# Performance work log

Measured on AMD Instinct MI355X. Metric: run time of the kernel, lower is better.

Reference implementation:

```python
import jax, jax.numpy as jnp
import numpy as np


def _freq_downsample(x, sf):
    # torch: stack(chunk(dim=2), 4) -> cat(chunk(dim=3), 4) -> mean(-1) -> repeat(1,1,sf,sf)
    # equivalent: mean over the sf x sf grid of contiguous blocks, then tile back.
    B, C, H, W = x.shape
    m = x.reshape(B, C, sf, H // sf, sf, W // sf).mean(axis=(2, 4))
    return jnp.tile(m, (1, 1, sf, sf))


def setup_inputs() -> dict:
    key = jax.random.key(0)
    k1, k2, k3 = jax.random.split(key, 3)
    shape = (4, 3, 256, 256)
    return {
        "STy": jax.random.normal(k1, shape, dtype=jnp.float32),
        "Fk_real": jax.random.normal(k2, shape, dtype=jnp.float32),
        "Fk_imag": jax.random.normal(k3, shape, dtype=jnp.float32),
        "sf": 2,
    }


def _forward(STy, Fk_real, Fk_imag, sf, num_iters=50, alpha=1e-6, gam=0.1):
    fft2 = lambda a: jnp.fft.fft2(a, axes=(-2, -1))
    ifft2 = lambda a: jnp.fft.ifft2(a, axes=(-2, -1))

    Fk = jax.lax.complex(Fk_real, Fk_imag)          # complex64 OTF
    FkC = jnp.conj(Fk)
    Fk2 = Fk_real ** 2 + Fk_imag ** 2               # |Fk|^2, real

    FSTy = fft2(STy)
    Fr = FkC * FSTy / (_freq_downsample(Fk2, sf) + alpha)
    pred = ifft2(Fr).real

    # finite-difference stencils DH = [1,-1] horizontal, DV vertical
    DH = jnp.zeros_like(pred).at[..., 0, 0].set(1.0).at[..., 0, 1].set(-1.0)
    DV = jnp.zeros_like(pred).at[..., 0, 0].set(1.0).at[..., 1, 0].set(-1.0)
    FDH, FDV = fft2(DH), fft2(DV)
    FDHC, FDVC = jnp.conj(FDH), jnp.conj(FDV)
    FD2 = jnp.abs(FDV) ** 2 + jnp.abs(FDH) ** 2 + 1e-8  # real

    # loop-invariant terms (identical math to recomputing each iteration)
    den = _freq_downsample(Fk2 / FD2, sf) + alpha
    FkFSTy = FkC * FSTy

    def body(carry, k):
        pred, x_old, t_old, U1, U2, D1, D2 = carry
        gam_k = gam * jnp.exp2(-k / num_iters)      # gam * 0.5 ** (k/num_iters)
        Fr = FkFSTy + alpha * (FDHC * fft2(U1 - D1) + FDVC * fft2(U2 - D2))
        Fr = (Fr - FkC * _freq_downsample(Fk * Fr / FD2, sf) / den) / (alpha * FD2)
        x_new = ifft2(Fr).real
        t_new = (1.0 + jnp.sqrt(1.0 + 4.0 * t_old ** 2)) / 2.0
        pred = x_new + (t_old - 1.0) / t_new * (x_new - x_old)
        DHr = ifft2(Fr * FDH).real
        DVr = ifft2(Fr * FDV).real
        NU1, NU2 = DHr + D1, DVr + D2
        NU = jnp.sqrt(NU1 ** 2 + NU2 ** 2 + 1e-8)
        A = jnp.maximum(0.0, NU - gam_k) + 1e-8
        A = A / (A + gam_k)                         # soft-threshold magnitude shrink
        U1n, U2n = A * NU1, A * NU2
        return (pred, x_new, t_new, U1n, U2n, D1 + DHr - U1n, D2 + DVr - U2n), None

    carry0 = (pred, pred, jnp.float32(1.0), pred, pred,
              jnp.zeros_like(pred), jnp.zeros_like(pred))
    ks = jnp.arange(num_iters, dtype=jnp.float32)
    (pred, *_), _ = jax.lax.scan(body, carry0, ks)
    return pred


def reference(STy, Fk_real, Fk_imag, sf):
    return _forward(STy, Fk_real, Fk_imag, sf)
```

## Files before the change

kernel.cpp:

```cpp
#include <hip/hip_runtime.h>
#include <math.h>

#define NIMG 12
#define NSZ 256
#define HWSZ 65536
#define NBLK 768

struct GBar { unsigned cnt; unsigned gen; };

__device__ __forceinline__ void gsync(GBar* b)
{
  __syncthreads();
  if (threadIdx.x == 0) {
    __threadfence();
    unsigned g = __hip_atomic_load(&b->gen, __ATOMIC_RELAXED, __HIP_MEMORY_SCOPE_AGENT);
    unsigned a = __hip_atomic_fetch_add(&b->cnt, 1u, __ATOMIC_ACQ_REL, __HIP_MEMORY_SCOPE_AGENT);
    if (a == NBLK - 1u) {
      __hip_atomic_store(&b->cnt, 0u, __ATOMIC_RELAXED, __HIP_MEMORY_SCOPE_AGENT);
      __hip_atomic_store(&b->gen, g + 1u, __ATOMIC_RELEASE, __HIP_MEMORY_SCOPE_AGENT);
    } else {
      while (__hip_atomic_load(&b->gen, __ATOMIC_ACQUIRE, __HIP_MEMORY_SCOPE_AGENT) == g)
        __builtin_amdgcn_s_sleep(2);
    }
    __threadfence();
  }
  __syncthreads();
}

__device__ __forceinline__ void fft256g(float2* A, float2* B, const float2* tw, int lane,
                                        float dir, bool active)
{
  float2* src = A;
  float2* dst = B;
  int m = 1;
#pragma unroll
  for (int s = 0; s < 8; ++s) {
    __syncthreads();
    if (active) {
#pragma unroll
      for (int h = 0; h < 2; ++h) {
        int b = lane + (h << 6);
        int k = b & (m - 1);
        int jm = b - k;
        float2 a = src[b];
        float2 c = src[b + 128];
        float2 w = tw[jm];
        float wr = w.x, wi = dir * w.y;
        float ex = a.x - c.x, ey = a.y - c.y;
        dst[2 * jm + k]     = make_float2(a.x + c.x, a.y + c.y);
        dst[2 * jm + k + m] = make_float2(ex * wr - ey * wi, ex * wi + ey * wr);
      }
    }
    float2* t = src; src = dst; dst = t;
    m <<= 1;
  }
  __syncthreads();
}
__device__ __forceinline__ void fft256(float2* A, float2* B, const float2* tw, int lane, float dir)
{
  fft256g(A, B, tw, lane, dir, true);
}

__device__ __forceinline__ void make_tw(float2* tw, int t)
{
  float s, c;
  sincospif((float)t * (1.0f / 128.0f), &s, &c);
  tw[t] = make_float2(c, s);
}

__device__ __forceinline__ double fdval(const float2* tw, int k)
{
  return 2.0 - 2.0 * (double)tw[k].x;
}

__global__ __launch_bounds__(256, 3) void k_mega(const float* __restrict__ sty,
                                                 const float* __restrict__ fkr,
                                                 const float* __restrict__ fki,
                                                 float2* __restrict__ WG,
                                                 float2* __restrict__ WF,
                                                 float2* __restrict__ FkF,
                                                 float* __restrict__ denq,
                                                 float* D1a, float* D2a,
                                                 float* D1b, float* D2b,
                                                 float* __restrict__ x49,
                                                 float* __restrict__ out,
                                                 float cmom, GBar* bar)
{
  __shared__ float2 tw[256];
  __shared__ float2 bufA[6][256];
  __shared__ float2 bufB[6][256];
  __shared__ float aL[5][256];
  __shared__ float bL[5][256];
  __shared__ float dsA[2][128];
  __shared__ double2 Ml[2][128];

  int t = threadIdx.x;
  make_tw(tw, t);
  int bid = blockIdx.x;
  int n = bid >> 6;
  int sr = bid & 63;
  int r0 = sr << 2;
  int j0 = sr << 1;
  int w = t >> 6, lane = t & 63;
  const float sc = 1.0f / 65536.0f;
  int gcw = j0 + (w & 1) + ((w >> 1) << 7);

  {
    const float* src = sty + (size_t)n * HWSZ + (size_t)(r0 + w) * NSZ;
#pragma unroll
    for (int q = 0; q < 4; ++q) { int j = lane + (q << 6); bufA[w][j] = make_float2(src[j], 0.f); }
    fft256(bufA[w], bufB[w], tw, lane, -1.f);
    float2* dst = WG + (size_t)n * HWSZ + (size_t)(r0 + w) * NSZ;
#pragma unroll
    for (int q = 0; q < 4; ++q) { int j = lane + (q << 6); dst[j] = bufA[w][j]; }
  }
  gsync(bar);

  {
    float2* WGn = WG + (size_t)n * HWSZ;
#pragma unroll
    for (int q = 0; q < 4; ++q) { int u = lane + (q << 6); bufA[w][u] = WGn[(size_t)u * NSZ + gcw]; }
    fft256(bufA[w], bufB[w], tw, lane, -1.f);
#pragma unroll
    for (int c = 0; c < 4; ++c) {
      int u = t;
      int gc = j0 + (c & 1) + ((c >> 1) << 7);
      size_t idx = (size_t)n * HWSZ + (size_t)u * NSZ + gc;
      float kr = fkr[idx], ki = fki[idx];
      float2 f = bufA[c][u];
      float2 kf = make_float2(kr * f.x + ki * f.y, kr * f.y - ki * f.x);
      FkF[idx] = kf;
      bufA[c][u] = kf;
    }
    __syncthreads();
    {
      int u0 = t & 127, p = t >> 7;
      double s1 = 0.0, s2 = 0.0;
#pragma unroll
      for (int s = 0; s < 4; ++s) {
        int u = u0 + ((s & 1) << 7);
        int c = p + ((s >> 1) << 1);
        int gc = j0 + (c & 1) + ((c >> 1) << 7);
        size_t idx = (size_t)n * HWSZ + (size_t)u * NSZ + gc;
        double kr = fkr[idx], ki = fki[idx];
        double k2 = kr * kr + ki * ki;
        double fd2 = fdval(tw, u) + fdval(tw, gc) + 1e-8;
        s1 += k2;
        s2 += k2 / fd2;
      }
      denq[(size_t)n * 16384 + (size_t)u0 * 128 + (j0 + p)] = (float)(s2 * 0.25 + 1e-6);
      dsA[p][u0] = (float)(s1 * 0.25 + 1e-6);
    }
    __syncthreads();
#pragma unroll
    for (int c = 0; c < 4; ++c) {
      int u = t;
      float d = dsA[c & 1][u & 127];
      float2 kf = bufA[c][u];
      bufA[c][u] = make_float2(kf.x / d, kf.y / d);
    }
    fft256(bufA[w], bufB[w], tw, lane, +1.f);
    float2* WFn = WF + (size_t)n * HWSZ;
#pragma unroll
    for (int q = 0; q < 4; ++q) { int u = lane + (q << 6); WFn[(size_t)u * NSZ + gcw] = bufA[w][u]; }
  }
  gsync(bar);

  for (int k = 0; k < 50; ++k) {
    float gamp = (k >= 1) ? (float)(0.1 * exp2(-(double)(k - 1) / 50.0)) : 0.f;
    const float *D1p, *D2p; float *D1w, *D2w;
    if (k & 1) { D1p = D1a; D2p = D2a; D1w = D1b; D2w = D2b; }
    else       { D1p = D1b; D2p = D2b; D1w = D1a; D2w = D2a; }

    {
      int gr = (r0 + w - 1) & 255;
      const float2* srcW = WF + (size_t)n * HWSZ + (size_t)gr * NSZ;
#pragma unroll
      for (int q = 0; q < 4; ++q) { int j = lane + (q << 6); bufA[w][j] = srcW[j]; }
      fft256(bufA[w], bufB[w], tw, lane, +1.f);
    }
    {
      bool act = (w < 2);
      int e = 4 + (w & 1);
      int gr = (r0 + e - 1) & 255;
      if (act) {
        const float2* srcW = WF + (size_t)n * HWSZ + (size_t)gr * NSZ;
#pragma unroll
        for (int q = 0; q < 4; ++q) { int j = lane + (q << 6); bufA[e][j] = srcW[j]; }
      }
      fft256g(bufA[e], bufB[e], tw, lane, +1.f, act);
    }
    for (int e = 1; e <= 5; ++e) {
      int gr = (r0 + e - 1) & 255;
      int j = t, jm1 = (j - 1) & 255;
      float xc = bufA[e][j].x * sc;
      size_t idx = (size_t)n * HWSZ + (size_t)gr * NSZ + j;
      if (k == 49 && e <= 4) x49[idx] = xc;
      float a, b;
      if (k == 0) {
        a = xc; b = xc;
      } else {
        float xl = bufA[e][jm1].x * sc;
        float xu = bufA[e - 1][j].x * sc;
        float dhr = xc - xl;
        float dvr = xc - xu;
        float d1 = D1p[idx], d2 = D2p[idx];
        float nu1 = dhr + d1, nu2 = dvr + d2;
        float nu = sqrtf(nu1 * nu1 + nu2 * nu2 + 1e-8f);
        float A = fmaxf(0.f, nu - gamp) + 1e-8f;
        A = A / (A + gamp);
        float u1 = A * nu1, u2 = A * nu2;
        float d1v = d1 + dhr - u1;
        float d2v = d2 + dvr - u2;
        if (e <= 4) { D1w[idx] = d1v; D2w[idx] = d2v; }
        a = u1 - d1v; b = u2 - d2v;
      }
      aL[e - 1][j] = a;
      bL[e - 1][j] = b;
    }
    __syncthreads();
    {
#pragma unroll
      for (int q = 0; q < 4; ++q) {
        int j = lane + (q << 6);
        int jp1 = (j + 1) & 255;
        float g = aL[w][j] - aL[w][jp1] + bL[w][j] - bL[w + 1][j];
        bufA[w][j] = make_float2(g, 0.f);
      }
      fft256(bufA[w], bufB[w], tw, lane, -1.f);
      float2* dst = WG + (size_t)n * HWSZ + (size_t)(r0 + w) * NSZ;
#pragma unroll
      for (int q = 0; q < 4; ++q) { int j = lane + (q << 6); dst[j] = bufA[w][j]; }
    }
    gsync(bar);

    {
      float2* WGn = WG + (size_t)n * HWSZ;
#pragma unroll
      for (int q = 0; q < 4; ++q) { int u = lane + (q << 6); bufA[w][u] = WGn[(size_t)u * NSZ + gcw]; }
      fft256(bufA[w], bufB[w], tw, lane, -1.f);
#pragma unroll
      for (int c = 0; c < 4; ++c) {
        int u = t;
        int gc = j0 + (c & 1) + ((c >> 1) << 7);
        size_t idx = (size_t)n * HWSZ + (size_t)u * NSZ + gc;
        float2 kf = FkF[idx];
        float2 fg = bufA[c][u];
        bufA[c][u] = make_float2(kf.x + 1e-6f * fg.x, kf.y + 1e-6f * fg.y);
      }
      __syncthreads();
      {
        int u0 = t & 127, p = t >> 7;
        double sx = 0.0, sy = 0.0;
#pragma unroll
        for (int s = 0; s < 4; ++s) {
          int u = u0 + ((s & 1) << 7);
          int c = p + ((s >> 1) << 1);
          int gc = j0 + (c & 1) + ((c >> 1) << 7);
          size_t idx = (size_t)n * HWSZ + (size_t)u * NSZ + gc;
          float2 f1 = bufA[c][u];
          double kr = fkr[idx], ki = fki[idx];
          double fd2 = fdval(tw, u) + fdval(tw, gc) + 1e-8;
          sx += (kr * (double)f1.x - ki * (double)f1.y) / fd2;
          sy += (kr * (double)f1.y + ki * (double)f1.x) / fd2;
        }
        Ml[p][u0] = make_double2(sx * 0.25, sy * 0.25);
      }
      __syncthreads();
#pragma unroll
      for (int c = 0; c < 4; ++c) {
        int u = t;
        int gc = j0 + (c & 1) + ((c >> 1) << 7);
        size_t idx = (size_t)n * HWSZ + (size_t)u * NSZ + gc;
        float2 f1 = bufA[c][u];
        double2 m = Ml[c & 1][u & 127];
        double den = (double)denq[(size_t)n * 16384 + (size_t)(u & 127) * 128 + (j0 + (c & 1))];
        double kr = fkr[idx], ki = fki[idx];
        double px = (kr * m.x + ki * m.y) / den;
        double py = (kr * m.y - ki * m.x) / den;
        double fd2 = fdval(tw, u) + fdval(tw, gc) + 1e-8;
        double s2 = 1.0 / (1e-6 * fd2);
        bufA[c][u] = make_float2((float)(((double)f1.x - px) * s2),
                                 (float)(((double)f1.y - py) * s2));
      }
      fft256(bufA[w], bufB[w], tw, lane, +1.f);
      float2* WFn = WF + (size_t)n * HWSZ;
#pragma unroll
      for (int q = 0; q < 4; ++q) { int u = lane + (q << 6); WFn[(size_t)u * NSZ + gcw] = bufA[w][u]; }
    }
    gsync(bar);
  }

  {
    const float2* srcW = WF + (size_t)n * HWSZ + (size_t)(r0 + w) * NSZ;
#pragma unroll
    for (int q = 0; q < 4; ++q) { int j = lane + (q << 6); bufA[w][j] = srcW[j]; }
    fft256(bufA[w], bufB[w], tw, lane, +1.f);
    size_t base = (size_t)n * HWSZ + (size_t)(r0 + w) * NSZ;
#pragma unroll
    for (int q = 0; q < 4; ++q) {
      int j = lane + (q << 6);
      float v = bufA[w][j].x * sc;
      out[base + j] = v + cmom * (v - x49[base + j]);
    }
  }
}

__global__ __launch_bounds__(256) void k_rowfwd_sty(const float* __restrict__ sty,
                                                    float2* __restrict__ Wb)
{
  __shared__ float2 tw[256];
  __shared__ float2 bufA[4][256];
  __shared__ float2 bufB[4][256];
  int t = threadIdx.x;
  make_tw(tw, t);
  int n = blockIdx.x >> 6;
  int r0 = (blockIdx.x & 63) << 2;
  int w = t >> 6, lane = t & 63;
  const float* src = sty + (size_t)n * HWSZ + (size_t)(r0 + w) * NSZ;
#pragma unroll
  for (int q = 0; q < 4; ++q) { int j = lane + (q << 6); bufA[w][j] = make_float2(src[j], 0.f); }
  fft256(bufA[w], bufB[w], tw, lane, -1.f);
  float2* dst = Wb + (size_t)n * HWSZ + (size_t)(r0 + w) * NSZ;
#pragma unroll
  for (int q = 0; q < 4; ++q) { int j = lane + (q << 6); dst[j] = bufA[w][j]; }
}

__global__ __launch_bounds__(256) void k_colsetup(float2* __restrict__ Wb,
                                                  float2* __restrict__ FkF,
                                                  const float* __restrict__ fkr,
                                                  const float* __restrict__ fki,
                                                  float* __restrict__ denq)
{
  __shared__ float2 tw[256];
  __shared__ float2 bufA[4][256];
  __shared__ float2 bufB[4][256];
  __shared__ float dsA[2][128];
  int t = threadIdx.x;
  make_tw(tw, t);
  int n = blockIdx.x >> 6;
  int j0 = (blockIdx.x & 63) << 1;
  int w = t >> 6, lane = t & 63;
  int gcw = j0 + (w & 1) + ((w >> 1) << 7);
  float2* Wn = Wb + (size_t)n * HWSZ;
#pragma unroll
  for (int q = 0; q < 4; ++q) { int u = lane + (q << 6); bufA[w][u] = Wn[(size_t)u * NSZ + gcw]; }
  fft256(bufA[w], bufB[w], tw, lane, -1.f);
#pragma unroll
  for (int c = 0; c < 4; ++c) {
    int u = t;
    int gc = j0 + (c & 1) + ((c >> 1) << 7);
    size_t idx = (size_t)n * HWSZ + (size_t)u * NSZ + gc;
    float kr = fkr[idx], ki = fki[idx];
    float2 f = bufA[c][u];
    float2 kf = make_float2(kr * f.x + ki * f.y, kr * f.y - ki * f.x);
    FkF[idx] = kf;
    bufA[c][u] = kf;
  }
  __syncthreads();
  {
    int u0 = t & 127, p = t >> 7;
    double s1 = 0.0, s2 = 0.0;
#pragma unroll
    for (int s = 0; s < 4; ++s) {
      int u = u0 + ((s & 1) << 7);
      int c = p + ((s >> 1) << 1);
      int gc = j0 + (c & 1) + ((c >> 1) << 7);
      size_t idx = (size_t)n * HWSZ + (size_t)u * NSZ + gc;
      double kr = fkr[idx], ki = fki[idx];
      double k2 = kr * kr + ki * ki;
      double fd2 = fdval(tw, u) + fdval(tw, gc) + 1e-8;
      s1 += k2;
      s2 += k2 / fd2;
    }
    denq[(size_t)n * 16384 + (size_t)u0 * 128 + (j0 + p)] = (float)(s2 * 0.25 + 1e-6);
    dsA[p][u0] = (float)(s1 * 0.25 + 1e-6);
  }
  __syncthreads();
#pragma unroll
  for (int c = 0; c < 4; ++c) {
    int u = t;
    float d = dsA[c & 1][u & 127];
    float2 kf = bufA[c][u];
    bufA[c][u] = make_float2(kf.x / d, kf.y / d);
  }
  fft256(bufA[w], bufB[w], tw, lane, +1.f);
#pragma unroll
  for (int q = 0; q < 4; ++q) { int u = lane + (q << 6); Wn[(size_t)u * NSZ + gcw] = bufA[w][u]; }
}

__global__ __launch_bounds__(256) void k_spatial_rowfwd(const float* __restrict__ x,
                                                        const float* __restrict__ D1p,
                                                        const float* __restrict__ D2p,
                                                        float* __restrict__ D1n,
                                                        float* __restrict__ D2n,
                                                        float2* __restrict__ Wb,
                                                        float gamp, int firstIter)
{
  __shared__ float2 tw[256];
  __shared__ float aL[5][256];
  __shared__ float bL[5][256];
  __shared__ float2 bufA[4][256];
  __shared__ float2 bufB[4][256];
  int t = threadIdx.x;
  make_tw(tw, t);
  int n = blockIdx.x >> 6;
  int r0 = (blockIdx.x & 63) << 2;
  const float* xn = x + (size_t)n * HWSZ;
  for (int rr = 0; rr < 5; ++rr) {
    int i = (r0 + rr) & 255;
    int im1 = (i - 1) & 255;
    int j = t;
    int jm1 = (j - 1) & 255;
    float xc = xn[(size_t)i * NSZ + j];
    float a, b;
    if (firstIter) {
      a = xc; b = xc;
    } else {
      float dhr = xc - xn[(size_t)i * NSZ + jm1];
      float dvr = xc - xn[(size_t)im1 * NSZ + j];
      size_t idx = (size_t)n * HWSZ + (size_t)i * NSZ + j;
      float d1 = D1p[idx], d2 = D2p[idx];
      float nu1 = dhr + d1, nu2 = dvr + d2;
      float nu = sqrtf(nu1 * nu1 + nu2 * nu2 + 1e-8f);
      float A = fmaxf(0.f, nu - gamp) + 1e-8f;
      A = A / (A + gamp);
      float u1 = A * nu1, u2 = A * nu2;
      float d1v = d1 + dhr - u1;
      float d2v = d2 + dvr - u2;
      if (rr < 4) { D1n[idx] = d1v; D2n[idx] = d2v; }
      a = u1 - d1v; b = u2 - d2v;
    }
    aL[rr][j] = a;
    bL[rr][j] = b;
  }
  __syncthreads();
  int w = t >> 6, lane = t & 63;
#pragma unroll
  for (int q = 0; q < 4; ++q) {
    int j = lane + (q << 6);
    int jp1 = (j + 1) & 255;
    float g = aL[w][j] - aL[w][jp1] + bL[w][j] - bL[w + 1][j];
    bufA[w][j] = make_float2(g, 0.f);
  }
  fft256(bufA[w], bufB[w], tw, lane, -1.f);
  float2* dst = Wb + (size_t)n * HWSZ + (size_t)(r0 + w) * NSZ;
#pragma unroll
  for (int q = 0; q < 4; ++q) { int j = lane + (q << 6); dst[j] = bufA[w][j]; }
}

__global__ __launch_bounds__(256) void k_colphase(float2* __restrict__ Wb,
                                                  const float2* __restrict__ FkF,
                                                  const float* __restrict__ fkr,
                                                  const float* __restrict__ fki,
                                                  const float* __restrict__ denq)
{
  __shared__ float2 tw[256];
  __shared__ float2 bufA[4][256];
  __shared__ float2 bufB[4][256];
  __shared__ double2 Ml[2][128];
  int t = threadIdx.x;
  make_tw(tw, t);
  int n = blockIdx.x >> 6;
  int j0 = (blockIdx.x & 63) << 1;
  int w = t >> 6, lane = t & 63;
  int gcw = j0 + (w & 1) + ((w >> 1) << 7);
  float2* Wn = Wb + (size_t)n * HWSZ;
#pragma unroll
  for (int q = 0; q < 4; ++q) { int u = lane + (q << 6); bufA[w][u] = Wn[(size_t)u * NSZ + gcw]; }
  fft256(bufA[w], bufB[w], tw, lane, -1.f);
#pragma unroll
  for (int c = 0; c < 4; ++c) {
    int u = t;
    int gc = j0 + (c & 1) + ((c >> 1) << 7);
    size_t idx = (size_t)n * HWSZ + (size_t)u * NSZ + gc;
    float2 kf = FkF[idx];
    float2 fg = bufA[c][u];
    bufA[c][u] = make_float2(kf.x + 1e-6f * fg.x, kf.y + 1e-6f * fg.y);
  }
  __syncthreads();
  {
    int u0 = t & 127, p = t >> 7;
    double sx = 0.0, sy = 0.0;
#pragma unroll
    for (int s = 0; s < 4; ++s) {
      int u = u0 + ((s & 1) << 7);
      int c = p + ((s >> 1) << 1);
      int gc = j0 + (c & 1) + ((c >> 1) << 7);
      size_t idx = (size_t)n * HWSZ + (size_t)u * NSZ + gc;
      float2 f1 = bufA[c][u];
      double kr = fkr[idx], ki = fki[idx];
      double fd2 = fdval(tw, u) + fdval(tw, gc) + 1e-8;
      sx += (kr * (double)f1.x - ki * (double)f1.y) / fd2;
      sy += (kr * (double)f1.y + ki * (double)f1.x) / fd2;
    }
    Ml[p][u0] = make_double2(sx * 0.25, sy * 0.25);
  }
  __syncthreads();
#pragma unroll
  for (int c = 0; c < 4; ++c) {
    int u = t;
    int gc = j0 + (c & 1) + ((c >> 1) << 7);
    size_t idx = (size_t)n * HWSZ + (size_t)u * NSZ + gc;
    float2 f1 = bufA[c][u];
    double2 m = Ml[c & 1][u & 127];
    double den = (double)denq[(size_t)n * 16384 + (size_t)(u & 127) * 128 + (j0 + (c & 1))];
    double kr = fkr[idx], ki = fki[idx];
    double px = (kr * m.x + ki * m.y) / den;
    double py = (kr * m.y - ki * m.x) / den;
    double fd2 = fdval(tw, u) + fdval(tw, gc) + 1e-8;
    double s2 = 1.0 / (1e-6 * fd2);
    bufA[c][u] = make_float2((float)(((double)f1.x - px) * s2),
                             (float)(((double)f1.y - py) * s2));
  }
  fft256(bufA[w], bufB[w], tw, lane, +1.f);
#pragma unroll
  for (int q = 0; q < 4; ++q) { int u = lane + (q << 6); Wn[(size_t)u * NSZ + gcw] = bufA[w][u]; }
}

__global__ __launch_bounds__(256) void k_rowinv(const float2* __restrict__ Wb,
                                                float* __restrict__ xout,
                                                const float* __restrict__ xold,
                                                float* __restrict__ pred,
                                                float cmom, int isLast)
{
  __shared__ float2 tw[256];
  __shared__ float2 bufA[4][256];
  __shared__ float2 bufB[4][256];
  int t = threadIdx.x;
  make_tw(tw, t);
  int n = blockIdx.x >> 6;
  int r0 = (blockIdx.x & 63) << 2;
  int w = t >> 6, lane = t & 63;
  const float2* src = Wb + (size_t)n * HWSZ + (size_t)(r0 + w) * NSZ;
#pragma unroll
  for (int q = 0; q < 4; ++q) { int j = lane + (q << 6); bufA[w][j] = src[j]; }
  fft256(bufA[w], bufB[w], tw, lane, +1.f);
  size_t base = (size_t)n * HWSZ + (size_t)(r0 + w) * NSZ;
#pragma unroll
  for (int q = 0; q < 4; ++q) {
    int j = lane + (q << 6);
    float v = bufA[w][j].x * (1.0f / 65536.0f);
    xout[base + j] = v;
    if (isLast) pred[base + j] = v + cmom * (v - xold[base + j]);
  }
}

extern "C" void kernel_launch(void* const* d_in, const int* in_sizes, int n_in,
                              void* d_out, int out_size, void* d_ws, size_t ws_size,
                              hipStream_t stream)
{
  (void)in_sizes; (void)n_in; (void)out_size; (void)ws_size;
  const float* STy = (const float*)d_in[0];
  const float* fkr = (const float*)d_in[1];
  const float* fki = (const float*)d_in[2];
  float* out = (float*)d_out;

  char* p = (char*)d_ws;
  const size_t cplx = (size_t)NIMG * HWSZ * sizeof(float2);
  const size_t realb = (size_t)NIMG * HWSZ * sizeof(float);
  float2* WG  = (float2*)p; p += cplx;
  float2* WF  = (float2*)p; p += cplx;
  float2* FkF = (float2*)p; p += cplx;
  float* denq = (float*)p;  p += (size_t)NIMG * 16384 * sizeof(float);
  float* D1a = (float*)p;   p += realb;
  float* D2a = (float*)p;   p += realb;
  float* D1b = (float*)p;   p += realb;
  float* D2b = (float*)p;   p += realb;
  float* xA  = (float*)p;   p += realb;
  float* xB  = (float*)p;   p += realb;
  GBar* bar  = (GBar*)p;    p += 64;

  double t_old = 1.0, cm = 0.0;
  for (int k = 0; k < 50; ++k) {
    double t_new = (1.0 + sqrt(1.0 + 4.0 * t_old * t_old)) * 0.5;
    if (k == 49) cm = (t_old - 1.0) / t_new;
    t_old = t_new;
  }

  int maxb = 0;
  hipError_t oe = hipOccupancyMaxActiveBlocksPerMultiprocessor(&maxb, k_mega, 256, 0);
  bool coop = (oe == hipSuccess && maxb >= 3);

  hipMemsetAsync(D1a, 0, 2 * realb, stream);

  dim3 grid(NBLK), blk(256);
  if (coop) {
    hipMemsetAsync(bar, 0, sizeof(GBar), stream);
    k_mega<<<grid, blk, 0, stream>>>(STy, fkr, fki, WG, WF, FkF, denq,
                                     D1a, D2a, D1b, D2b, xA, out, (float)cm, bar);
  } else {
    float2* Wb = WG;
    float* x0 = xA; float* x1 = xB;
    k_rowfwd_sty<<<grid, blk, 0, stream>>>(STy, Wb);
    k_colsetup<<<grid, blk, 0, stream>>>(Wb, FkF, fkr, fki, denq);
    k_rowinv<<<grid, blk, 0, stream>>>(Wb, x0, x0, out, 0.f, 0);
    double to = 1.0;
    for (int k = 0; k < 50; ++k) {
      float gamp = (k >= 1) ? (float)(0.1 * exp2(-(double)(k - 1) / 50.0)) : 0.f;
      const float* xk = (k & 1) ? x1 : x0;
      float* xn = (k & 1) ? x0 : x1;
      const float* D1p = (k & 1) ? D1a : D1b;
      const float* D2p = (k & 1) ? D2a : D2b;
      float* D1w = (k & 1) ? D1b : D1a;
      float* D2w = (k & 1) ? D2b : D2a;
      k_spatial_rowfwd<<<grid, blk, 0, stream>>>(xk, D1p, D2p, D1w, D2w, Wb, gamp, (k == 0) ? 1 : 0);
      k_colphase<<<grid, blk, 0, stream>>>(Wb, FkF, fkr, fki, denq);
      double tn = (1.0 + sqrt(1.0 + 4.0 * to * to)) * 0.5;
      int isLast = (k == 49) ? 1 : 0;
      float cmom = (float)((to - 1.0) / tn);
      k_rowinv<<<grid, blk, 0, stream>>>(Wb, xn, xk, out, isLast ? cmom : 0.f, isLast);
      to = tn;
    }
  }
}
```

Baseline: 2.499 ms.

## Replace global grid barrier with per-image flag barriers

Swaps the single grid-wide counter barrier for a per-image barrier. Each of the 64 blocks working on an image publishes a generation flag, and one wavefront polls all 64 flags of that image. Images no longer wait on each other, and contention on a single atomic counter goes away. This relies on each image's data dependencies being confined to its own 64 blocks, and it adds polling traffic on 64 flags per block.

```diff
diff --git a/kernel.cpp b/kernel.cpp
--- a/kernel.cpp
+++ b/kernel.cpp
@@ -6,23 +6,20 @@
 #define HWSZ 65536
 #define NBLK 768
 
-struct GBar { unsigned cnt; unsigned gen; };
-
-__device__ __forceinline__ void gsync(GBar* b)
-{
-  __syncthreads();
-  if (threadIdx.x == 0) {
-    __threadfence();
-    unsigned g = __hip_atomic_load(&b->gen, __ATOMIC_RELAXED, __HIP_MEMORY_SCOPE_AGENT);
-    unsigned a = __hip_atomic_fetch_add(&b->cnt, 1u, __ATOMIC_ACQ_REL, __HIP_MEMORY_SCOPE_AGENT);
-    if (a == NBLK - 1u) {
-      __hip_atomic_store(&b->cnt, 0u, __ATOMIC_RELAXED, __HIP_MEMORY_SCOPE_AGENT);
-      __hip_atomic_store(&b->gen, g + 1u, __ATOMIC_RELEASE, __HIP_MEMORY_SCOPE_AGENT);
-    } else {
-      while (__hip_atomic_load(&b->gen, __ATOMIC_ACQUIRE, __HIP_MEMORY_SCOPE_AGENT) == g)
-        __builtin_amdgcn_s_sleep(2);
-    }
-    __threadfence();
+__device__ __forceinline__ void isync(unsigned* flags, int base, int sr, unsigned gen)
+{
+  __syncthreads();
+  int t = threadIdx.x;
+  if (t < 64) {
+    if (t == 0) {
+      __builtin_amdgcn_fence(__ATOMIC_RELEASE, "agent");
+      __hip_atomic_store(&flags[base + sr], gen, __ATOMIC_RELAXED, __HIP_MEMORY_SCOPE_AGENT);
+    }
+    unsigned v;
+    do {
+      v = __hip_atomic_load(&flags[base + t], __ATOMIC_RELAXED, __HIP_MEMORY_SCOPE_AGENT);
+    } while (__any(v < gen));
+    __builtin_amdgcn_fence(__ATOMIC_ACQUIRE, "agent");
   }
   __syncthreads();
 }
@@ -84,7 +81,7 @@
                                                  float* D1b, float* D2b,
                                                  float* __restrict__ x49,
                                                  float* __restrict__ out,
-                                                 float cmom, GBar* bar)
+                                                 float cmom, unsigned* flags)
 {
   __shared__ float2 tw[256];
   __shared__ float2 bufA[6][256];
@@ -99,11 +96,13 @@
   int bid = blockIdx.x;
   int n = bid >> 6;
   int sr = bid & 63;
+  int fbase = n << 6;
   int r0 = sr << 2;
   int j0 = sr << 1;
   int w = t >> 6, lane = t & 63;
   const float sc = 1.0f / 65536.0f;
   int gcw = j0 + (w & 1) + ((w >> 1) << 7);
+  unsigned gen = 0;
 
   {
     const float* src = sty + (size_t)n * HWSZ + (size_t)(r0 + w) * NSZ;
@@ -114,7 +113,7 @@
 #pragma unroll
     for (int q = 0; q < 4; ++q) { int j = lane + (q << 6); dst[j] = bufA[w][j]; }
   }
-  gsync(bar);
+  isync(flags, fbase, sr, ++gen);
 
   {
     float2* WGn = WG + (size_t)n * HWSZ;
@@ -164,7 +163,7 @@
 #pragma unroll
     for (int q = 0; q < 4; ++q) { int u = lane + (q << 6); WFn[(size_t)u * NSZ + gcw] = bufA[w][u]; }
   }
-  gsync(bar);
+  isync(flags, fbase, sr, ++gen);
 
   for (int k = 0; k < 50; ++k) {
     float gamp = (k >= 1) ? (float)(0.1 * exp2(-(double)(k - 1) / 50.0)) : 0.f;
@@ -232,7 +231,7 @@
 #pragma unroll
       for (int q = 0; q < 4; ++q) { int j = lane + (q << 6); dst[j] = bufA[w][j]; }
     }
-    gsync(bar);
+    isync(flags, fbase, sr, ++gen);
 
     {
       float2* WGn = WG + (size_t)n * HWSZ;
@@ -288,7 +287,7 @@
 #pragma unroll
       for (int q = 0; q < 4; ++q) { int u = lane + (q << 6); WFn[(size_t)u * NSZ + gcw] = bufA[w][u]; }
     }
-    gsync(bar);
+    isync(flags, fbase, sr, ++gen);
   }
 
   {
@@ -569,7 +568,7 @@
   float* D2b = (float*)p;   p += realb;
   float* xA  = (float*)p;   p += realb;
   float* xB  = (float*)p;   p += realb;
-  GBar* bar  = (GBar*)p;    p += 64;
+  unsigned* flags = (unsigned*)p; p += 4096;
 
   double t_old = 1.0, cm = 0.0;
   for (int k = 0; k < 50; ++k) {
@@ -586,9 +585,9 @@
 
   dim3 grid(NBLK), blk(256);
   if (coop) {
-    hipMemsetAsync(bar, 0, sizeof(GBar), stream);
+    hipMemsetAsync(flags, 0, 4096, stream);
     k_mega<<<grid, blk, 0, stream>>>(STy, fkr, fki, WG, WF, FkF, denq,
-                                     D1a, D2a, D1b, D2b, xA, out, (float)cm, bar);
+                                     D1a, D2a, D1b, D2b, xA, out, (float)cm, flags);
   } else {
     float2* Wb = WG;
     float* x0 = xA; float* x1 = xB;
```

Result: no change. 2.485 ms (-0.5%).
